# Performance work log

Measured on AMD Instinct MI355X. Metric: run time of the kernel, lower is better.

Reference implementation:

```python
import jax, jax.numpy as jnp
import numpy as np

# graph structure constants (uniform graphs => simple coloring / masks all-true)
G, NV, EPG, LEPG = 128, 32, 64, 256          # graphs, nodes/graph, g-edges/graph, lg-edges/graph
NG, NLG, ELG, K = G * NV, G * EPG, G * LEPG, EPG  # K = n_colors = lg-nodes per graph
H, HF, T, L, NC, FIN, FE, NB = 32, 128, 8, 4, 12, 16, 16, 4  # hidden, hidden_final, towers, layers, classes, node feats, edge feats, basis

_FLOATS = ('x_g','edge_attr_g','x_lg','edge_attr_lg','W_enc','b_enc','W_msg','b_msg','W_init','b_init','np_l1_w','np_l1_b','np_l2_w','np_l2_b','np_lin_w','np_lin_b','fe_l1_w','fe_l1_b','fe_l2_w','fe_l2_b','fe_lin_w','fe_lin_b','gd_w','gd_b','ga_w','ga_b','ld_w','ld_b','la_w','la_b','u1_w','u1_b','u2_w','u2_b','u3_w','u3_b','en_w','en_b','li_w','li_b','lj_w','lj_b','bn_g','bn_b','ac_w','ac_b','fl_w','fl_b')

def _lin(x, w, b):
    return x @ w + b

def _glin(x, w, b):
    # grouped (tower) linear: w [T, c, c], block-diagonal over channel groups
    t, ci, co = w.shape
    y = jnp.einsum('...tc,tcd->...td', x.reshape(x.shape[:-1] + (t, ci)), w)
    return y.reshape(x.shape[:-1] + (t * co,)) + b

def setup_inputs():
    rng = np.random.default_rng(0)
    off_n = np.arange(G)[:, None] * NV
    ei_g = np.stack([(rng.integers(0, NV, (G, EPG)) + off_n).ravel(),
                     (rng.integers(0, NV, (G, EPG)) + off_n).ravel()])
    off_e = np.arange(G)[:, None] * EPG
    ei_lg = np.stack([(rng.integers(0, EPG, (G, LEPG)) + off_e).ravel(),
                      (rng.integers(0, EPG, (G, LEPG)) + off_e).ravel()])
    keys = iter(jax.random.split(jax.random.key(0), 64))
    def nrm(shape, fan):
        return (jax.random.normal(next(keys), shape, dtype=jnp.float32) / np.float32(np.sqrt(fan)))
    z = lambda *s: jnp.zeros(s, jnp.float32)
    inp = {
        'x_g': nrm((NG, FIN), 1.0),
        'edge_attr_g': nrm((NLG, FE), 1.0),
        'x_lg': nrm((NLG, NB), 1.0),
        'edge_attr_lg': nrm((ELG, NB), 1.0),
        'W_enc': nrm((FIN, H), FIN), 'b_enc': z(H),
        'W_msg': nrm((2 * H + FE + NB, HF), 2 * H + FE + NB), 'b_msg': z(HF),
        'W_init': nrm((HF + 1, H), HF + 1), 'b_init': z(H),
        'np_l1_w': nrm((HF + 1, HF), HF + 1), 'np_l1_b': z(HF),
        'np_l2_w': nrm((HF + 1, HF), HF + 1), 'np_l2_b': z(HF),
        'np_lin_w': nrm((HF, HF), HF), 'np_lin_b': z(HF),
        'fe_l1_w': nrm((H, HF), H), 'fe_l1_b': z(HF),
        'fe_l2_w': nrm((H, HF), H), 'fe_l2_b': z(HF),
        'fe_lin_w': nrm((HF, HF), HF), 'fe_lin_b': z(HF),
        'gd_w': nrm((NB, NB), NB), 'gd_b': z(NB),
        'ga_w': nrm((NB, NB), NB), 'ga_b': z(NB),
        'ld_w': nrm((L, NB, H), NB), 'ld_b': z(L, H),
        'la_w': nrm((L, NB, H), NB), 'la_b': z(L, H),
        'u1_w': nrm((L, T, H // T, H // T), H // T), 'u1_b': z(L, H),
        'u2_w': nrm((L, T, H // T, H // T), H // T), 'u2_b': z(L, H),
        'u3_w': nrm((L, T, H // T, H // T), H // T), 'u3_b': z(L, H),
        'en_w': nrm((L, H, H), H), 'en_b': z(L, H),
        'li_w': nrm((L, T, H // T, H // T), H // T), 'li_b': z(L, H),
        'lj_w': nrm((L, T, H // T, H // T), H // T), 'lj_b': z(L, H),
        'bn_g': jnp.ones((L, H), jnp.float32), 'bn_b': z(L, H),
        'ac_w': nrm((HF, HF), HF), 'ac_b': z(HF),
        'fl_w': nrm((HF, NC), HF), 'fl_b': z(NC),
        'edge_index_g': jnp.asarray(ei_g, dtype=jnp.int32),
        'edge_index_lg': jnp.asarray(ei_lg, dtype=jnp.int32),
        'batch_g': jnp.asarray(np.repeat(np.arange(G), NV), dtype=jnp.int32),
    }
    return inp

def _forward(fl, edge_index_g, edge_index_lg, batch_g):
    p = dict(zip(_FLOATS, fl))
    h = _lin(p['x_g'], p['W_enc'], p['b_enc'])                                 # [NG, H]
    s, d = edge_index_g[0], edge_index_g[1]
    hm = _lin(jnp.concatenate([h[s], h[d], p['edge_attr_g'], p['x_lg']], -1),
              p['W_msg'], p['b_msg'])                                          # [NLG, HF]
    batch_lg = batch_g[s]                                                      # graph id per lg node
    coloring = jnp.arange(NLG, dtype=jnp.int32) - batch_lg * EPG               # local color in [0, K)
    onehot = (coloring[:, None] == jnp.arange(K)).astype(hm.dtype)             # [NLG, K]
    # map_x_to_u: one-hot identity channel + features on own color row
    u = jnp.concatenate([onehot[:, :, None], onehot[:, :, None] * hm[:, None, :]], 2)  # [NLG, K, HF+1]
    edge_glob = _lin(p['edge_attr_lg'], p['ga_w'], p['ga_b'])                  # [ELG, NB]
    dist_glob = _lin(p['x_lg'], p['gd_w'], p['gd_b'])                          # [NLG, NB]
    ls, ld = edge_index_lg[0], edge_index_lg[1]
    indeg = jax.ops.segment_sum(jnp.ones((ELG,), hm.dtype), ld, num_segments=NLG)
    avg_e = (jax.ops.segment_sum(indeg, batch_lg, num_segments=G) / EPG)[batch_lg]  # avg edges/graph per node
    idx = jnp.arange(NLG)
    nb = jnp.asarray(EPG, hm.dtype)                                            # lg nodes per graph

    def extract(u, w1, b1, w2, b2, lw, lb):
        # GraphExtractor: UtoGlobal (mean-over-colors pool + diagonal pool) + residual relu lin
        mean = jax.ops.segment_sum(u.sum(1) / nb, batch_lg, num_segments=G) / nb
        diag = jax.ops.segment_sum(u[idx, coloring], batch_lg, num_segments=G) / nb
        out = _lin(mean, w1, b1) + _lin(diag, w2, b2)
        return out + jax.nn.relu(_lin(out, lw, lb))

    out = extract(u, p['np_l1_w'], p['np_l1_b'], p['np_l2_w'], p['np_l2_b'], p['np_lin_w'], p['np_lin_b'])
    u = _lin(u, p['W_init'], p['b_init'])                                      # [NLG, K, H]
    for i in range(L):
        if i > 0:  # batch norm (training-mode stats over nodes x colors)
            m = u.mean((0, 1)); v = u.var((0, 1))
            u = (u - m) * jax.lax.rsqrt(v + 1e-5) * p['bn_g'][i] + p['bn_b'][i]
        dist_loc = _lin(dist_glob, p['ld_w'][i], p['ld_b'][i])                 # [NLG, H]
        edge_loc = _lin(edge_glob, p['la_w'][i], p['la_b'][i])                 # [ELG, H]
        # SMPLayer: UtoU message net (entrywise + color-mean + diagonal terms, towered)
        um = (_glin(u, p['u1_w'][i], p['u1_b'][i])
              + _glin(u.sum(1) / nb, p['u2_w'][i], p['u2_b'][i])[:, None, :]
              + _glin(u[idx, coloring], p['u3_w'][i], p['u3_b'][i])[:, None, :])
        um = um * dist_loc[:, None, :]                                         # distance-basis filter
        ui = _glin(um, p['li_w'][i], p['li_b'][i])
        uj = _glin(um, p['lj_w'][i], p['lj_b'][i])
        ef = _lin(edge_loc, p['en_w'][i], p['en_b'][i])[:, None, :]
        msg = um[ls] + jax.nn.relu(ui[ld] + uj[ls] + ef)                       # [ELG, K, H]
        u = jax.ops.segment_sum(msg, ld, num_segments=NLG) / avg_e[:, None, None] + u
        out = out + extract(u, p['fe_l1_w'], p['fe_l1_b'], p['fe_l2_w'], p['fe_l2_b'], p['fe_lin_w'], p['fe_lin_b']) / L
    out = jax.nn.relu(_lin(out, p['ac_w'], p['ac_b'])) + out
    return _lin(out, p['fl_w'], p['fl_b'])                                     # [G, NC]

def reference(x_g, edge_attr_g, x_lg, edge_attr_lg, W_enc, b_enc, W_msg, b_msg, W_init, b_init, np_l1_w, np_l1_b, np_l2_w, np_l2_b, np_lin_w, np_lin_b, fe_l1_w, fe_l1_b, fe_l2_w, fe_l2_b, fe_lin_w, fe_lin_b, gd_w, gd_b, ga_w, ga_b, ld_w, ld_b, la_w, la_b, u1_w, u1_b, u2_w, u2_b, u3_w, u3_b, en_w, en_b, li_w, li_b, lj_w, lj_b, bn_g, bn_b, ac_w, ac_b, fl_w, fl_b, edge_index_g, edge_index_lg, batch_g):
    args = dict(locals())
    fl = tuple(args[n] for n in _FLOATS)
    return _forward(fl, edge_index_g, edge_index_lg, batch_g)
```

## Files before the change

kernel.cpp:

```cpp
#include <hip/hip_runtime.h>

#define G_    128
#define NV_   32
#define EPG_  64
#define LEPG_ 256
#define NG_   (G_*NV_)
#define NLG_  (G_*EPG_)
#define ELG_  (G_*LEPG_)
#define K_    64
#define H_    32
#define HF_   128
#define L_    4
#define NC_   12
#define FIN_  16
#define FE_   16
#define NB_   4
#define TILE_ (K_*H_)

__global__ __launch_bounds__(256) void kA(
    const float* __restrict__ xg, const float* __restrict__ Wenc,
    const float* __restrict__ benc,
    const float* __restrict__ ealg, const float* __restrict__ gaw,
    const float* __restrict__ gab,
    const float* __restrict__ xlg, const float* __restrict__ gdw,
    const float* __restrict__ gdb,
    const float* __restrict__ eag, const float* __restrict__ Wm,
    const float* __restrict__ bm,
    const int* __restrict__ ls, const int* __restrict__ ldst,
    float* __restrict__ h, float* __restrict__ eglob, float* __restrict__ dglob,
    float* __restrict__ p1, float* __restrict__ p2, float* __restrict__ q34,
    int* __restrict__ offsg, int* __restrict__ csrp, float* __restrict__ bna)
{
    __shared__ int cnt[64], offs[65], cur[64];
    int bid = blockIdx.x, t = threadIdx.x;
    if (bid == 0) {
        bna[t] = 0.f;
        return;
    }
    if (bid < 1 + 1152) {
        int lb = bid - 1;
        if (lb < 512) {
            int gid = lb*256 + t; int nn = gid>>5, ch = gid&31;
            float s = benc[ch];
#pragma unroll
            for (int f = 0; f < FIN_; ++f) s += xg[nn*FIN_+f]*Wenc[f*H_+ch];
            h[gid] = s;
        } else {
            int gid = (lb-512)*256 + t;
            if (gid < ELG_*4) {
                int e = gid>>2, k = gid&3;
                float s = gab[k];
#pragma unroll
                for (int j = 0; j < 4; ++j) s += ealg[e*4+j]*gaw[j*4+k];
                eglob[gid] = s;
            } else {
                int gid2 = gid - ELG_*4;
                int nn = gid2>>2, k = gid2&3;
                float s = gdb[k];
#pragma unroll
                for (int j = 0; j < 4; ++j) s += xlg[nn*4+j]*gdw[j*4+k];
                dglob[gid2] = s;
            }
        }
        return;
    }
    if (bid < 1 + 1152 + 2048) {
        int lb = bid - 1153;
        int n = lb*2 + (t>>7), o = t&127;
        float hv[32];
#pragma unroll
        for (int k = 0; k < 32; ++k) {
            float s = benc[k];
#pragma unroll
            for (int f = 0; f < FIN_; ++f) s += xg[n*FIN_+f]*Wenc[f*H_+k];
            hv[k] = s;
        }
        float a = 0.f, b = 0.f;
#pragma unroll
        for (int k = 0; k < 32; ++k) {
            a += hv[k] * Wm[k*HF_ + o];
            b += hv[k] * Wm[(32+k)*HF_ + o];
        }
        p1[n*HF_ + o] = a; p2[n*HF_ + o] = b;
        return;
    }
    if (bid < 1 + 1152 + 2048 + 4096) {
        int lb = bid - 3201;
        int e = lb*2 + (t>>7), o = t&127;
        float s = bm[o];
#pragma unroll
        for (int k = 0; k < 16; ++k) s += eag[e*16+k] * Wm[(64+k)*HF_ + o];
#pragma unroll
        for (int k = 0; k < 4; ++k)  s += xlg[e*4+k]  * Wm[(80+k)*HF_ + o];
        q34[e*HF_ + o] = s;
        return;
    }
    {
        int g = bid - 7297;
        if (t < 64) cnt[t] = 0;
        __syncthreads();
        int d = ldst[g*256 + t] & 63;
        int sl = ls[g*256 + t] & 63;
        atomicAdd(&cnt[d], 1);
        __syncthreads();
        if (t == 0) {
            int a = 0;
            for (int i = 0; i < 64; ++i) { offs[i] = a; a += cnt[i]; }
            offs[64] = a;
        }
        __syncthreads();
        if (t < 64) { cur[t] = offs[t]; offsg[g*65 + t] = offs[t]; }
        if (t == 0) offsg[g*65 + 64] = offs[64];
        __syncthreads();
        int p = atomicAdd(&cur[d], 1);
        csrp[g*256 + p] = (t << 6) | sl;
    }
}

__global__ __launch_bounds__(256) void kB(
    const float* __restrict__ p1, const float* __restrict__ p2,
    const float* __restrict__ q34, const int* __restrict__ sidx,
    const int* __restrict__ didx, float* __restrict__ hm,
    const float* __restrict__ dgl, const float* __restrict__ egl,
    const float* __restrict__ ldw, const float* __restrict__ ldb,
    const float* __restrict__ law, const float* __restrict__ lab,
    const float* __restrict__ enw, const float* __restrict__ enb,
    float* __restrict__ dlb, float* __restrict__ efb)
{
    __shared__ float el[8][32];
    int bid = blockIdx.x, t = threadIdx.x;
    if (bid < 1024) {
        int idx = bid*256 + t;
        int e = idx >> 5, o4 = idx & 31;
        int s = sidx[e], d = didx[e];
        float4 a = ((const float4*)p1)[s*32 + o4];
        float4 b = ((const float4*)p2)[d*32 + o4];
        float4 q = ((const float4*)q34)[e*32 + o4];
        ((float4*)hm)[idx] = make_float4(a.x+b.x+q.x, a.y+b.y+q.y, a.z+b.z+q.z, a.w+b.w+q.w);
        return;
    }
    int lb = bid - 1024;
    if (lb < 4096) {
        int gid = lb*256 + t;
        int l = gid >> 18, rem = gid & ((1<<18)-1);
        int n = rem >> 5, ch = rem & 31;
        float s = ldb[l*32 + ch];
#pragma unroll
        for (int j = 0; j < 4; ++j) s += dgl[n*4+j] * ldw[l*128 + j*32 + ch];
        dlb[gid] = s;
    } else {
        int p = (lb - 4096)*8 + (t >> 5);
        int ch = t & 31;
        int l = p >> 15, e = p & 32767;
        float s = lab[l*32 + ch];
#pragma unroll
        for (int j = 0; j < 4; ++j) s += egl[e*4+j] * law[l*128 + j*32 + ch];
        el[t>>5][ch] = s;
        __syncthreads();
        float o = enb[l*32 + ch];
        for (int k = 0; k < 32; ++k) o += el[t>>5][k] * enw[l*1024 + k*32 + ch];
        efb[(size_t)l*ELG_*32 + e*32 + ch] = o;
    }
}

__global__ __launch_bounds__(256) void kC(
    const float* __restrict__ hm, const float* __restrict__ Wi,
    const float* __restrict__ bi, float* __restrict__ rv,
    float* __restrict__ cs, float* __restrict__ ds,
    const float* __restrict__ l1w, const float* __restrict__ l1b,
    const float* __restrict__ l2w, const float* __restrict__ l2b,
    const float* __restrict__ lnw, const float* __restrict__ lnb,
    float* __restrict__ out_acc)
{
    __shared__ float mh[128], o1[128];
    int bid = blockIdx.x, t = threadIdx.x;
    if (bid < 1024) {
        int n = bid*8 + (t>>5), ch = t&31;
        float s = Wi[ch];
        for (int f = 0; f < HF_; ++f) s += hm[n*HF_ + f] * Wi[(1+f)*H_ + ch];
        rv[n*32 + ch] = s;
        cs[n*32 + ch] = 64.f*bi[ch] + s;
        ds[n*32 + ch] = bi[ch] + s;
        return;
    }
    int g = bid - 1024;
    if (t < 128) {
        float s = 0.f;
        for (int k = 0; k < 64; ++k) s += hm[(g*64+k)*HF_ + t];
        mh[t] = s * (1.f/64.f);
    }
    __syncthreads();
    float o = 0.f;
    if (t < 128) {
        o = l1b[t] + l2b[t] + (l1w[t]*(1.f/64.f) + l2w[t]);
        for (int k = 0; k < 128; ++k)
            o += mh[k] * (l1w[(1+k)*HF_ + t]*(1.f/64.f) + l2w[(1+k)*HF_ + t]);
        o1[t] = o;
    }
    __syncthreads();
    if (t < 128) {
        float r = lnb[t];
        for (int k = 0; k < 128; ++k) r += o1[k] * lnw[k*HF_ + t];
        out_acc[g*HF_ + t] = o + (r > 0.f ? r : 0.f);
    }
}

__global__ __launch_bounds__(256) void k_gtdl(
    const float* __restrict__ cs, const float* __restrict__ ds,
    const float* __restrict__ bnaP, const float* __restrict__ bng,
    const float* __restrict__ bnb, int lay,
    const float* __restrict__ u1w, const float* __restrict__ u2w,
    const float* __restrict__ u3w, const float* __restrict__ u1b,
    const float* __restrict__ u2b, const float* __restrict__ u3b,
    const float* __restrict__ dl_l, float* __restrict__ gtb) {
    int idx = blockIdx.x*256 + threadIdx.x;
    int n = idx >> 5, ch = idx & 31;
    int chi = ch & 3, twb = ch & ~3;
    float gt = u1b[ch] + u2b[ch] + u3b[ch];
#pragma unroll
    for (int j = 0; j < 4; ++j) {
        int bj = twb + j;
        float s_ = 1.f, sh_ = 0.f;
        if (lay > 0) {
            float m = bnaP[bj] * (1.f/524288.f);
            float v = bnaP[32+bj] * (1.f/524288.f) - m*m;
            s_ = bng[bj] * rsqrtf(v + 1e-5f);
            sh_ = bnb[bj] - m*s_;
        }
        float csF = s_*cs[n*32 + bj] + 64.f*sh_;
        float dgF = s_*ds[n*32 + bj] + sh_;
        gt += csF*(1.f/64.f)*u2w[bj*4 + chi] + dgF*u3w[bj*4 + chi]
            + sh_*u1w[bj*4 + chi];
    }
    gtb[idx] = gt * dl_l[idx];
}

#define PROC_NODE(ACC, UI, JE)                                              \
  for (; j < (JE); ++j) {                                                   \
    int jn = j + 2; jn = jn < 255 ? jn : 255;                               \
    int pkN = ep[jn];                                                       \
    float4 efN = *(const float4*)(ef_l + (((size_t)((g<<8)+(pkN>>6)))<<5) + chb); \
    int src = pkA & 63;                                                     \
    float4 u4 = *(float4*)&um[src*128 + coff];                              \
    float r0 = UI.x + efA.x + blj4[0] + u4.x*wj[0] + u4.y*wj[4] + u4.z*wj[8] + u4.w*wj[12]; \
    float r1 = UI.y + efA.y + blj4[1] + u4.x*wj[1] + u4.y*wj[5] + u4.z*wj[9] + u4.w*wj[13]; \
    float r2 = UI.z + efA.z + blj4[2] + u4.x*wj[2] + u4.y*wj[6] + u4.z*wj[10] + u4.w*wj[14]; \
    float r3 = UI.w + efA.w + blj4[3] + u4.x*wj[3] + u4.y*wj[7] + u4.z*wj[11] + u4.w*wj[15]; \
    ACC.x += u4.x + (r0>0.f?r0:0.f);                                        \
    ACC.y += u4.y + (r1>0.f?r1:0.f);                                        \
    ACC.z += u4.z + (r2>0.f?r2:0.f);                                        \
    ACC.w += u4.w + (r3>0.f?r3:0.f);                                        \
    pkA = pkB; efA = efB; pkB = pkN; efB = efN;                             \
  }

#define UM_NODE(I, UIOUT, DL, GT)                                           \
  {                                                                         \
    int nl = nq*4 + I;                                                      \
    float4 uv = *(float4*)&us[nl*128 + coff];                               \
    float m0 = (uv.x*w1f[0]+uv.y*w1f[4]+uv.z*w1f[8] +uv.w*w1f[12])*DL.x + GT.x; \
    float m1 = (uv.x*w1f[1]+uv.y*w1f[5]+uv.z*w1f[9] +uv.w*w1f[13])*DL.y + GT.y; \
    float m2 = (uv.x*w1f[2]+uv.y*w1f[6]+uv.z*w1f[10]+uv.w*w1f[14])*DL.z + GT.z; \
    float m3 = (uv.x*w1f[3]+uv.y*w1f[7]+uv.z*w1f[11]+uv.w*w1f[15])*DL.w + GT.w; \
    *(float4*)&um[nl*128 + coff] = make_float4(m0,m1,m2,m3);                \
    UIOUT.x = bli4[0] + m0*wi[0] + m1*wi[4] + m2*wi[8]  + m3*wi[12];        \
    UIOUT.y = bli4[1] + m0*wi[1] + m1*wi[5] + m2*wi[9]  + m3*wi[13];        \
    UIOUT.z = bli4[2] + m0*wi[2] + m1*wi[6] + m2*wi[10] + m3*wi[14];        \
    UIOUT.w = bli4[3] + m0*wi[3] + m1*wi[7] + m2*wi[11] + m3*wi[15];        \
  }

#define UN_NODE(I, ACC)                                                     \
  {                                                                         \
    float4 uo4 = *(float4*)&us[(nq*4+I)*128 + coff];                        \
    float4 un4;                                                             \
    un4.x = ACC.x*0.25f + sc4[0]*uo4.x + sh4[0];                            \
    un4.y = ACC.y*0.25f + sc4[1]*uo4.y + sh4[1];                            \
    un4.z = ACC.z*0.25f + sc4[2]*uo4.z + sh4[2];                            \
    un4.w = ACC.w*0.25f + sc4[3]*uo4.w + sh4[3];                            \
    if (!last)                                                              \
        *(float4*)(u_out + (((size_t)(n0g+I))<<11) + (ck<<7) + coff) = un4; \
    if (nq == ck && c == I)                                                 \
        *(float4*)&dsb[(((size_t)(n0g+I))<<5) + chb] = un4;                 \
    float cx=un4.x, cy=un4.y, cz=un4.z, cw=un4.w;                           \
    float qx=cx*cx, qy=cy*cy, qz=cz*cz, qw=cw*cw;                           \
    cx+=__shfl_xor(cx,8);  cy+=__shfl_xor(cy,8);  cz+=__shfl_xor(cz,8);  cw+=__shfl_xor(cw,8); \
    qx+=__shfl_xor(qx,8);  qy+=__shfl_xor(qy,8);  qz+=__shfl_xor(qz,8);  qw+=__shfl_xor(qw,8); \
    cx+=__shfl_xor(cx,16); cy+=__shfl_xor(cy,16); cz+=__shfl_xor(cz,16); cw+=__shfl_xor(cw,16); \
    qx+=__shfl_xor(qx,16); qy+=__shfl_xor(qy,16); qz+=__shfl_xor(qz,16); qw+=__shfl_xor(qw,16); \
    if (c == 0) {                                                           \
        *(float4*)&pcs[(((size_t)(ck*NLG_ + n0g + I))<<5) + chb] = make_float4(cx,cy,cz,cw); \
        *(float4*)&pss[(((size_t)(ck*NLG_ + n0g + I))<<5) + chb] = make_float4(qx,qy,qz,qw); \
    }                                                                       \
  }

__global__ __launch_bounds__(512, 4) void k_layer(
    const float* __restrict__ u_in, float* __restrict__ u_out,
    const int* __restrict__ offsg, const int* __restrict__ csrp,
    const float* __restrict__ bnaP, const float* __restrict__ bng,
    const float* __restrict__ bnb, int lay, int last,
    const float* __restrict__ rvb, const float* __restrict__ bi,
    const float* __restrict__ u1w,
    const float* __restrict__ liw, const float* __restrict__ lib,
    const float* __restrict__ ljw, const float* __restrict__ ljb,
    const float* __restrict__ dl_l, const float* __restrict__ gtb,
    const float* __restrict__ ef_l,
    float* __restrict__ pcs, float* __restrict__ pss, float* __restrict__ dsb)
{
    __shared__ float us[64*128];
    __shared__ float um[64*128];
    __shared__ int ep[256];
    __shared__ int offs[65];

    const int bid = blockIdx.x, t = threadIdx.x;
    const int g  = ((bid >> 7) << 3) | (bid & 7);
    const int ck = (bid >> 3) & 15;
    const int tw = t & 7, c = (t >> 3) & 3, nq = t >> 5;
    const int chb = tw * 4;
    const int coff = c*32 + chb;
    const int n0g = g*64 + nq*4;

    if (t < 256) ep[t] = csrp[g*256 + t];
    else if (t < 256 + 65) offs[t - 256] = offsg[g*65 + (t - 256)];

    if (lay == 0) {
#pragma unroll
        for (int r = 0; r < 4; ++r) {
            int lin = r*2048 + t*4;
            int nl = lin >> 7, off = lin & 127;
            int ch0 = off & 31, cw = off >> 5;
            float4 v = *(const float4*)(bi + ch0);
            if (ck*4 + cw == nl) {
                float4 rv4 = *(const float4*)(rvb + (size_t)(g*64 + nl)*32 + ch0);
                v.x += rv4.x; v.y += rv4.y; v.z += rv4.z; v.w += rv4.w;
            }
            *(float4*)&us[lin] = v;
        }
    } else {
        const float* ub = u_in + ((size_t)g << 17) + (ck << 7);
#pragma unroll
        for (int r = 0; r < 4; ++r) {
            int lin = r*2048 + t*4;
            int nl = lin >> 7, off = lin & 127;
            float4 v = *(const float4*)(ub + ((size_t)nl << 11) + off);
            *(float4*)&us[lin] = v;
        }
    }

    float4 dl0 = *(const float4*)(dl_l + (((size_t)(n0g+0))<<5) + chb);
    float4 dl1 = *(const float4*)(dl_l + (((size_t)(n0g+1))<<5) + chb);
    float4 dl2 = *(const float4*)(dl_l + (((size_t)(n0g+2))<<5) + chb);
    float4 dl3 = *(const float4*)(dl_l + (((size_t)(n0g+3))<<5) + chb);
    float4 gt0 = *(const float4*)(gtb + (((size_t)(n0g+0))<<5) + chb);
    float4 gt1 = *(const float4*)(gtb + (((size_t)(n0g+1))<<5) + chb);
    float4 gt2 = *(const float4*)(gtb + (((size_t)(n0g+2))<<5) + chb);
    float4 gt3 = *(const float4*)(gtb + (((size_t)(n0g+3))<<5) + chb);

    float sc4[4], sh4[4];
    if (lay > 0) {
#pragma unroll
        for (int j2 = 0; j2 < 4; ++j2) {
            int bj = chb + j2;
            float m = bnaP[bj] * (1.f/524288.f);
            float v = bnaP[32+bj] * (1.f/524288.f) - m*m;
            float s_ = bng[bj] * rsqrtf(v + 1e-5f);
            sc4[j2] = s_; sh4[j2] = bnb[bj] - m*s_;
        }
    } else {
#pragma unroll
        for (int j2 = 0; j2 < 4; ++j2) { sc4[j2] = 1.f; sh4[j2] = 0.f; }
    }
    float w1f[16], wi[16], wj[16], bli4[4], blj4[4];
#pragma unroll
    for (int j2 = 0; j2 < 4; ++j2)
#pragma unroll
        for (int d = 0; d < 4; ++d) {
            w1f[j2*4+d] = u1w[(chb+j2)*4 + d] * sc4[j2];
            wi [j2*4+d] = liw[(chb+j2)*4 + d];
            wj [j2*4+d] = ljw[(chb+j2)*4 + d];
        }
#pragma unroll
    for (int d = 0; d < 4; ++d) { bli4[d] = lib[chb+d]; blj4[d] = ljb[chb+d]; }

    __syncthreads();

    float4 ui0, ui1, ui2, ui3;
    UM_NODE(0, ui0, dl0, gt0)
    UM_NODE(1, ui1, dl1, gt1)
    UM_NODE(2, ui2, dl2, gt2)
    UM_NODE(3, ui3, dl3, gt3)
    __syncthreads();

    float4 acc0 = make_float4(0,0,0,0), acc1 = acc0, acc2 = acc0, acc3 = acc0;
    int j = offs[nq*4];
    {
        int ja = j < 255 ? j : 255;
        int pkA = ep[ja];
        float4 efA = *(const float4*)(ef_l + (((size_t)((g<<8)+(pkA>>6)))<<5) + chb);
        int jb = (j+1) < 255 ? (j+1) : 255;
        int pkB = ep[jb];
        float4 efB = *(const float4*)(ef_l + (((size_t)((g<<8)+(pkB>>6)))<<5) + chb);
        int e1 = offs[nq*4+1], e2 = offs[nq*4+2], e3 = offs[nq*4+3], e4 = offs[nq*4+4];
        PROC_NODE(acc0, ui0, e1)
        PROC_NODE(acc1, ui1, e2)
        PROC_NODE(acc2, ui2, e3)
        PROC_NODE(acc3, ui3, e4)
    }

    UN_NODE(0, acc0)
    UN_NODE(1, acc1)
    UN_NODE(2, acc2)
    UN_NODE(3, acc3)
}

__global__ __launch_bounds__(256) void k_midx(
    const float* __restrict__ pcs, const float* __restrict__ pss,
    const float* __restrict__ dsb,
    const float* __restrict__ l1w, const float* __restrict__ l1b,
    const float* __restrict__ l2w, const float* __restrict__ l2b,
    const float* __restrict__ lnw, const float* __restrict__ lnb,
    float* __restrict__ csb, float* __restrict__ bna_i,
    float* __restrict__ out_acc, float scale,
    int do_final, const float* __restrict__ acw, const float* __restrict__ acb,
    const float* __restrict__ flw, const float* __restrict__ flb,
    float* __restrict__ outp)
{
    __shared__ float red[3*128];
    __shared__ float S[32], D[32], o1[128], ov[128], t1[128];
    int g = blockIdx.x, t = threadIdx.x;
    int ch = t & 31, ng = t >> 5;
    float pS = 0.f, pQ = 0.f, pD = 0.f;
#pragma unroll
    for (int k = 0; k < 8; ++k) {
        int n = g*64 + ng + 8*k;
        float cs_ = 0.f, ss_ = 0.f;
#pragma unroll
        for (int ckk = 0; ckk < 16; ++ckk) {
            cs_ += pcs[((size_t)ckk*NLG_ + n)*32 + ch];
            ss_ += pss[((size_t)ckk*NLG_ + n)*32 + ch];
        }
        csb[n*32 + ch] = cs_;
        pS += cs_; pQ += ss_;
        pD += dsb[n*32 + ch];
    }
    pS += __shfl_xor(pS, 32); pQ += __shfl_xor(pQ, 32); pD += __shfl_xor(pD, 32);
    int w = t >> 6;
    if ((t & 63) < 32) {
        red[w*32 + ch] = pS;
        red[128 + w*32 + ch] = pQ;
        red[256 + w*32 + ch] = pD;
    }
    __syncthreads();
    if (t < 32) {
        float S_ = 0.f, Q_ = 0.f, D_ = 0.f;
#pragma unroll
        for (int ww = 0; ww < 4; ++ww) {
            S_ += red[ww*32 + t]; Q_ += red[128 + ww*32 + t]; D_ += red[256 + ww*32 + t];
        }
        S[t] = S_; D[t] = D_;
        atomicAdd(&bna_i[t], S_);
        atomicAdd(&bna_i[32 + t], Q_);
    }
    __syncthreads();
    float o = 0.f;
    if (t < 128) {
        o = l1b[t] + l2b[t];
        for (int k = 0; k < 32; ++k)
            o += (S[k]*(1.f/4096.f))*l1w[k*HF_ + t] + (D[k]*(1.f/64.f))*l2w[k*HF_ + t];
        o1[t] = o;
    }
    __syncthreads();
    if (t < 128) {
        float r = lnb[t];
        for (int k = 0; k < 128; ++k) r += o1[k] * lnw[k*HF_ + t];
        float newv = out_acc[g*HF_ + t] + (o + (r > 0.f ? r : 0.f)) * scale;
        out_acc[g*HF_ + t] = newv;
        ov[t] = newv;
    }
    if (do_final) {
        __syncthreads();
        if (t < 128) {
            float r2 = acb[t];
            for (int k = 0; k < 128; ++k) r2 += ov[k] * acw[k*HF_ + t];
            t1[t] = ov[t] + (r2 > 0.f ? r2 : 0.f);
        }
        __syncthreads();
        if (t < NC_) {
            float s2 = flb[t];
            for (int k = 0; k < 128; ++k) s2 += t1[k] * flw[k*NC_ + t];
            outp[g*NC_ + t] = s2;
        }
    }
}

extern "C" void kernel_launch(void* const* d_in, const int* in_sizes, int n_in,
                              void* d_out, int out_size, void* d_ws, size_t ws_size,
                              hipStream_t stream) {
    const float* x_g      = (const float*)d_in[0];
    const float* eag      = (const float*)d_in[1];
    const float* x_lg     = (const float*)d_in[2];
    const float* ealg     = (const float*)d_in[3];
    const float* W_enc    = (const float*)d_in[4];
    const float* b_enc    = (const float*)d_in[5];
    const float* W_msg    = (const float*)d_in[6];
    const float* b_msg    = (const float*)d_in[7];
    const float* W_init   = (const float*)d_in[8];
    const float* b_init   = (const float*)d_in[9];
    const float* np_l1_w  = (const float*)d_in[10];
    const float* np_l1_b  = (const float*)d_in[11];
    const float* np_l2_w  = (const float*)d_in[12];
    const float* np_l2_b  = (const float*)d_in[13];
    const float* np_lin_w = (const float*)d_in[14];
    const float* np_lin_b = (const float*)d_in[15];
    const float* fe_l1_w  = (const float*)d_in[16];
    const float* fe_l1_b  = (const float*)d_in[17];
    const float* fe_l2_w  = (const float*)d_in[18];
    const float* fe_l2_b  = (const float*)d_in[19];
    const float* fe_lin_w = (const float*)d_in[20];
    const float* fe_lin_b = (const float*)d_in[21];
    const float* gd_w     = (const float*)d_in[22];
    const float* gd_b     = (const float*)d_in[23];
    const float* ga_w     = (const float*)d_in[24];
    const float* ga_b     = (const float*)d_in[25];
    const float* ld_w     = (const float*)d_in[26];
    const float* ld_b     = (const float*)d_in[27];
    const float* la_w     = (const float*)d_in[28];
    const float* la_b     = (const float*)d_in[29];
    const float* u1_w     = (const float*)d_in[30];
    const float* u1_b     = (const float*)d_in[31];
    const float* u2_w     = (const float*)d_in[32];
    const float* u2_b     = (const float*)d_in[33];
    const float* u3_w     = (const float*)d_in[34];
    const float* u3_b     = (const float*)d_in[35];
    const float* en_w     = (const float*)d_in[36];
    const float* en_b     = (const float*)d_in[37];
    const float* li_w     = (const float*)d_in[38];
    const float* li_b     = (const float*)d_in[39];
    const float* lj_w     = (const float*)d_in[40];
    const float* lj_b     = (const float*)d_in[41];
    const float* bn_g     = (const float*)d_in[42];
    const float* bn_b     = (const float*)d_in[43];
    const float* ac_w     = (const float*)d_in[44];
    const float* ac_b     = (const float*)d_in[45];
    const float* fl_w     = (const float*)d_in[46];
    const float* fl_b     = (const float*)d_in[47];
    const int*   ei_g     = (const int*)d_in[48];
    const int*   ei_lg    = (const int*)d_in[49];

    const int* s_g  = ei_g;
    const int* d_g  = ei_g + NLG_;
    const int* ls   = ei_lg;
    const int* ldst = ei_lg + ELG_;

    float* ws = (float*)d_ws;
    size_t o = 0;
    float* ub0  = ws + o; o += (size_t)NLG_ * TILE_;
    float* ub1  = ws + o; o += (size_t)NLG_ * TILE_;
    float* hm   = ws + o; o += (size_t)NLG_ * HF_;
    float* hbuf = ws + o; o += (size_t)NG_ * H_;
    float* dgl  = ws + o; o += (size_t)NLG_ * NB_;
    float* egl  = ws + o; o += (size_t)ELG_ * NB_;
    float* p1b  = ws + o; o += (size_t)NG_ * HF_;
    float* p2b  = ws + o; o += (size_t)NG_ * HF_;
    float* q34b = ws + o; o += (size_t)NLG_ * HF_;
    float* rvb  = ws + o; o += (size_t)NLG_ * 32;
    float* csb  = ws + o; o += (size_t)NLG_ * 32;
    float* dsb  = ws + o; o += (size_t)NLG_ * 32;
    float* gtb  = ws + o; o += (size_t)NLG_ * 32;
    float* pcs  = ws + o; o += (size_t)16 * NLG_ * 32;
    float* pss  = ws + o; o += (size_t)16 * NLG_ * 32;
    float* oac  = ws + o; o += (size_t)G_ * HF_;
    float* bna  = ws + o; o += 256;
    float* dlb  = ws + o; o += (size_t)L_ * NLG_ * 32;
    float* efb  = ws + o; o += (size_t)L_ * ELG_ * 32;
    int*   offsg = (int*)(ws + o); o += G_ * 65;
    int*   csrp  = (int*)(ws + o); o += ELG_;

    kA<<<7425, 256, 0, stream>>>(x_g, W_enc, b_enc, ealg, ga_w, ga_b,
                                 x_lg, gd_w, gd_b, eag, W_msg, b_msg,
                                 ls, ldst,
                                 hbuf, egl, dgl, p1b, p2b, q34b,
                                 offsg, csrp, bna);
    kB<<<21504, 256, 0, stream>>>(p1b, p2b, q34b, s_g, d_g, hm,
                                  dgl, egl, ld_w, ld_b, la_w, la_b,
                                  en_w, en_b, dlb, efb);
    kC<<<1152, 256, 0, stream>>>(hm, W_init, b_init, rvb, csb, dsb,
                                 np_l1_w, np_l1_b, np_l2_w, np_l2_b,
                                 np_lin_w, np_lin_b, oac);

    float* ubufs[2] = {ub0, ub1};
    for (int i = 0; i < L_; ++i) {
        const float* ui = ubufs[i & 1];
        float* uo = ubufs[(i + 1) & 1];
        k_gtdl<<<1024, 256, 0, stream>>>(
            csb, dsb,
            (i > 0 ? bna + (i-1)*64 : bna), bn_g + i*32, bn_b + i*32, i,
            u1_w + i*128, u2_w + i*128, u3_w + i*128,
            u1_b + i*32, u2_b + i*32, u3_b + i*32,
            dlb + (size_t)i*NLG_*32, gtb);
        k_layer<<<2048, 512, 0, stream>>>(
            ui, uo, offsg, csrp,
            (i > 0 ? bna + (i-1)*64 : bna), bn_g + i*32, bn_b + i*32, i,
            (i == L_ - 1) ? 1 : 0,
            rvb, b_init,
            u1_w + i*128,
            li_w + i*128, li_b + i*32,
            lj_w + i*128, lj_b + i*32,
            dlb + (size_t)i*NLG_*32, gtb, efb + (size_t)i*ELG_*32,
            pcs, pss, dsb);
        k_midx<<<G_, 256, 0, stream>>>(
            pcs, pss, dsb,
            fe_l1_w, fe_l1_b, fe_l2_w, fe_l2_b, fe_lin_w, fe_lin_b,
            csb, bna + i*64, oac, 1.0f / (float)L_,
            (i == L_ - 1) ? 1 : 0, ac_w, ac_b, fl_w, fl_b, (float*)d_out);
    }
}
```

Before: 575.4 us.

## Merge us/um shared buffers into one and transpose partial-sum layout

```diff
diff --git a/kernel.cpp b/kernel.cpp
--- a/kernel.cpp
+++ b/kernel.cpp
@@ -241,7 +241,7 @@
     int pkN = ep[jn];                                                       \
     float4 efN = *(const float4*)(ef_l + (((size_t)((g<<8)+(pkN>>6)))<<5) + chb); \
     int src = pkA & 63;                                                     \
-    float4 u4 = *(float4*)&um[src*128 + coff];                              \
+    float4 u4 = *(float4*)&ub[src*128 + coff];                              \
     float r0 = UI.x + efA.x + blj4[0] + u4.x*wj[0] + u4.y*wj[4] + u4.z*wj[8] + u4.w*wj[12]; \
     float r1 = UI.y + efA.y + blj4[1] + u4.x*wj[1] + u4.y*wj[5] + u4.z*wj[9] + u4.w*wj[13]; \
     float r2 = UI.z + efA.z + blj4[2] + u4.x*wj[2] + u4.y*wj[6] + u4.z*wj[10] + u4.w*wj[14]; \
@@ -256,12 +256,12 @@
 #define UM_NODE(I, UIOUT, DL, GT)                                           \
   {                                                                         \
     int nl = nq*4 + I;                                                      \
-    float4 uv = *(float4*)&us[nl*128 + coff];                               \
+    float4 uv = *(float4*)&ub[nl*128 + coff];                               \
     float m0 = (uv.x*w1f[0]+uv.y*w1f[4]+uv.z*w1f[8] +uv.w*w1f[12])*DL.x + GT.x; \
     float m1 = (uv.x*w1f[1]+uv.y*w1f[5]+uv.z*w1f[9] +uv.w*w1f[13])*DL.y + GT.y; \
     float m2 = (uv.x*w1f[2]+uv.y*w1f[6]+uv.z*w1f[10]+uv.w*w1f[14])*DL.z + GT.z; \
     float m3 = (uv.x*w1f[3]+uv.y*w1f[7]+uv.z*w1f[11]+uv.w*w1f[15])*DL.w + GT.w; \
-    *(float4*)&um[nl*128 + coff] = make_float4(m0,m1,m2,m3);                \
+    *(float4*)&ub[nl*128 + coff] = make_float4(m0,m1,m2,m3);                \
     UIOUT.x = bli4[0] + m0*wi[0] + m1*wi[4] + m2*wi[8]  + m3*wi[12];        \
     UIOUT.y = bli4[1] + m0*wi[1] + m1*wi[5] + m2*wi[9]  + m3*wi[13];        \
     UIOUT.z = bli4[2] + m0*wi[2] + m1*wi[6] + m2*wi[10] + m3*wi[14];        \
@@ -270,7 +270,16 @@
 
 #define UN_NODE(I, ACC)                                                     \
   {                                                                         \
-    float4 uo4 = *(float4*)&us[(nq*4+I)*128 + coff];                        \
+    float4 uo4;                                                             \
+    if (lay == 0) {                                                         \
+        uo4 = bi4c;                                                         \
+        if (ck*4 + c == nq*4 + I) {                                         \
+            float4 rv4 = *(const float4*)(rvb + (size_t)(n0g+I)*32 + chb);  \
+            uo4.x += rv4.x; uo4.y += rv4.y; uo4.z += rv4.z; uo4.w += rv4.w; \
+        }                                                                   \
+    } else {                                                                \
+        uo4 = *(const float4*)(u_in + (((size_t)(n0g+I))<<11) + (ck<<7) + coff); \
+    }                                                                       \
     float4 un4;                                                             \
     un4.x = ACC.x*0.25f + sc4[0]*uo4.x + sh4[0];                            \
     un4.y = ACC.y*0.25f + sc4[1]*uo4.y + sh4[1];                            \
@@ -287,8 +296,8 @@
     cx+=__shfl_xor(cx,16); cy+=__shfl_xor(cy,16); cz+=__shfl_xor(cz,16); cw+=__shfl_xor(cw,16); \
     qx+=__shfl_xor(qx,16); qy+=__shfl_xor(qy,16); qz+=__shfl_xor(qz,16); qw+=__shfl_xor(qw,16); \
     if (c == 0) {                                                           \
-        *(float4*)&pcs[(((size_t)(ck*NLG_ + n0g + I))<<5) + chb] = make_float4(cx,cy,cz,cw); \
-        *(float4*)&pss[(((size_t)(ck*NLG_ + n0g + I))<<5) + chb] = make_float4(qx,qy,qz,qw); \
+        *(float4*)&pcs[(((size_t)(n0g+I))*16 + ck)*32 + chb] = make_float4(cx,cy,cz,cw); \
+        *(float4*)&pss[(((size_t)(n0g+I))*16 + ck)*32 + chb] = make_float4(qx,qy,qz,qw); \
     }                                                                       \
   }
 
@@ -305,8 +314,7 @@
     const float* __restrict__ ef_l,
     float* __restrict__ pcs, float* __restrict__ pss, float* __restrict__ dsb)
 {
-    __shared__ float us[64*128];
-    __shared__ float um[64*128];
+    __shared__ float ub[64*128];
     __shared__ int ep[256];
     __shared__ int offs[65];
 
@@ -332,16 +340,16 @@
                 float4 rv4 = *(const float4*)(rvb + (size_t)(g*64 + nl)*32 + ch0);
                 v.x += rv4.x; v.y += rv4.y; v.z += rv4.z; v.w += rv4.w;
             }
-            *(float4*)&us[lin] = v;
+            *(float4*)&ub[lin] = v;
         }
     } else {
-        const float* ub = u_in + ((size_t)g << 17) + (ck << 7);
+        const float* ugp = u_in + ((size_t)g << 17) + (ck << 7);
 #pragma unroll
         for (int r = 0; r < 4; ++r) {
             int lin = r*2048 + t*4;
             int nl = lin >> 7, off = lin & 127;
-            float4 v = *(const float4*)(ub + ((size_t)nl << 11) + off);
-            *(float4*)&us[lin] = v;
+            float4 v = *(const float4*)(ugp + ((size_t)nl << 11) + off);
+            *(float4*)&ub[lin] = v;
         }
     }
 
@@ -368,6 +376,7 @@
 #pragma unroll
         for (int j2 = 0; j2 < 4; ++j2) { sc4[j2] = 1.f; sh4[j2] = 0.f; }
     }
+    float4 bi4c = (lay == 0) ? *(const float4*)(bi + chb) : make_float4(0.f,0.f,0.f,0.f);
     float w1f[16], wi[16], wj[16], bli4[4], blj4[4];
 #pragma unroll
     for (int j2 = 0; j2 < 4; ++j2)
@@ -430,12 +439,15 @@
     float pS = 0.f, pQ = 0.f, pD = 0.f;
 #pragma unroll
     for (int k = 0; k < 8; ++k) {
-        int n = g*64 + ng + 8*k;
+        int nl = ng + 8*k;
+        int n = g*64 + nl;
+        const float* pc = pcs + ((size_t)n*16)*32 + ch;
+        const float* ps = pss + ((size_t)n*16)*32 + ch;
         float cs_ = 0.f, ss_ = 0.f;
 #pragma unroll
         for (int ckk = 0; ckk < 16; ++ckk) {
-            cs_ += pcs[((size_t)ckk*NLG_ + n)*32 + ch];
-            ss_ += pss[((size_t)ckk*NLG_ + n)*32 + ch];
+            cs_ += pc[ckk*32];
+            ss_ += ps[ckk*32];
         }
         csb[n*32 + ch] = cs_;
         pS += cs_; pQ += ss_;
```

Result: slower. 609.4 us (+5.9%).
